# Performance work log

Measured on AMD Instinct MI355X. Metric: run time of the kernel, lower is better.

The kernel has to match this reference:

```python
import jax, jax.numpy as jnp
import numpy as np

N_NODES = 100000
N_EDGES = 1000000
HID = 128


def setup_inputs() -> dict:
    key = jax.random.key(0)
    ks = jax.random.split(key, 6)
    x = jax.random.normal(ks[0], (N_NODES, HID), dtype=jnp.float32)
    edge_index = jax.random.randint(ks[1], (2, N_EDGES), 0, N_NODES, dtype=jnp.int32)
    edge_attr = jax.random.uniform(ks[2], (N_EDGES, 1), dtype=jnp.float32)
    # MLP params (PyTorch Linear default-ish init scale)
    d_in = 2 * HID + 1  # 257
    W1 = jax.random.normal(ks[3], (d_in, HID), dtype=jnp.float32) / np.sqrt(d_in)
    b1 = jnp.zeros((HID,), dtype=jnp.float32)
    W2 = jax.random.normal(ks[4], (HID, 32), dtype=jnp.float32) / np.sqrt(HID)
    b2 = jnp.zeros((32,), dtype=jnp.float32)
    W3 = jax.random.normal(ks[5], (32, 1), dtype=jnp.float32) / np.sqrt(32.0)
    b3 = jnp.zeros((1,), dtype=jnp.float32)
    return {"x": x, "edge_index": edge_index, "edge_attr": edge_attr,
            "W1": W1, "b1": b1, "W2": W2, "b2": b2, "W3": W3, "b3": b3}


def reference(x, edge_index, edge_attr, W1, b1, W2, b2, W3, b3):
    src = edge_index[0]
    dst = edge_index[1]
    # [E, 2*H+1] gather + concat
    ef = jnp.concatenate([x[src], x[dst], edge_attr], axis=1)
    h = jax.nn.relu(ef @ W1 + b1)          # [E, H] (dropout = identity in eval)
    h = jax.nn.relu(h @ W2 + b2)           # [E, 32]
    out = jax.nn.sigmoid(h @ W3 + b3)      # [E, 1]
    return out[:, 0]                        # [E]
```

## Files before the change

kernel.cpp:

```cpp
#include <hip/hip_runtime.h>

#define E_EDGES 1000000
#define NNODES  100000
#define HID     128
#define NG      31250
#define NBLK    768
#define NT      62500
#define EBLK    1536
#define PBLK    512

typedef float f32x4 __attribute__((ext_vector_type(4)));
typedef short s16x8 __attribute__((ext_vector_type(8)));

typedef __attribute__((address_space(3))) unsigned int lds_u32;
typedef const __attribute__((address_space(1))) unsigned int glb_u32;

__device__ __forceinline__ void gl_lds16(const void* g, void* l) {
  __builtin_amdgcn_global_load_lds((glb_u32*)g, (lds_u32*)l, 16, 0, 0);
}

__device__ __forceinline__ unsigned short f2bf(float f) {
  unsigned int u = __float_as_uint(f);
  u += 0x7FFFu + ((u >> 16) & 1u);
  return (unsigned short)(u >> 16);
}

__device__ __forceinline__ unsigned int cvtpk_bf16(float lo, float hi) {
  unsigned int r;
  asm("v_cvt_pk_bf16_f32 %0, %1, %2" : "=v"(r) : "v"(lo), "v"(hi));
  return r;
}

__device__ __forceinline__ float bflo(unsigned int u) {
  return __uint_as_float(u << 16);
}
__device__ __forceinline__ float bfhi(unsigned int u) {
  return __uint_as_float(u & 0xffff0000u);
}

__device__ __forceinline__ int4 pack8(float4 a, float4 b) {
  int4 v;
  v.x = (int)((unsigned)f2bf(a.x) | ((unsigned)f2bf(a.y) << 16));
  v.y = (int)((unsigned)f2bf(a.z) | ((unsigned)f2bf(a.w) << 16));
  v.z = (int)((unsigned)f2bf(b.x) | ((unsigned)f2bf(b.y) << 16));
  v.w = (int)((unsigned)f2bf(b.z) | ((unsigned)f2bf(b.w) << 16));
  return v;
}

__global__ void cast_x_kernel(const float* __restrict__ x,
                              unsigned short* __restrict__ xb) {
  int i = blockIdx.x * blockDim.x + threadIdx.x;
  const float4* p = (const float4*)x;
  float4 a = p[2 * i];
  float4 b = p[2 * i + 1];
  int4 v = pack8(a, b);
  ((int4*)xb)[i] = v;
}

__global__ void edge_naive(const float* __restrict__ x, const int* __restrict__ ei,
                           const float* __restrict__ attr, const float* __restrict__ W1,
                           const float* __restrict__ b1, const float* __restrict__ W2,
                           const float* __restrict__ b2, const float* __restrict__ W3,
                           const float* __restrict__ b3, float* __restrict__ out) {
  const int e = blockIdx.x * blockDim.x + threadIdx.x;
  if (e >= E_EDGES) return;
  const float* xs = x + (size_t)ei[e] * HID;
  const float* xd = x + (size_t)ei[E_EDGES + e] * HID;
  const float a = attr[e];
  float h1[HID];
  for (int n = 0; n < HID; ++n) {
    float s = b1[n] + a * W1[256 * HID + n];
    for (int k = 0; k < HID; ++k)
      s += xs[k] * W1[k * HID + n] + xd[k] * W1[(128 + k) * HID + n];
    h1[n] = fmaxf(s, 0.f);
  }
  float o = b3[0];
  for (int n2 = 0; n2 < 32; ++n2) {
    float s = b2[n2];
    for (int n = 0; n < HID; ++n) s += h1[n] * W2[n * 32 + n2];
    o += fmaxf(s, 0.f) * W3[n2];
  }
  out[e] = 1.f / (1.f + __expf(-o));
}

__launch_bounds__(256, 3)
__global__ void edge_mlp_kernel(const unsigned short* __restrict__ xb,
                                const int* __restrict__ ei,
                                const float* __restrict__ attr,
                                const float* __restrict__ W1,
                                const float* __restrict__ b1,
                                const float* __restrict__ W2,
                                const float* __restrict__ b2,
                                const float* __restrict__ W3,
                                const float* __restrict__ b3,
                                float* __restrict__ out) {
  __shared__ __align__(16) unsigned char ef[2][16384];
  __shared__ __align__(16) unsigned char h1b[2][8704];
  __shared__ float red[2][4][16];

  const int tid  = threadIdx.x;
  const int w    = tid >> 6;
  const int lane = tid & 63;
  const int q    = lane >> 4;
  const int l15  = lane & 15;

  s16x8 B1[2][8];
  float b1v[2], w1l[2];
#pragma unroll
  for (int th = 0; th < 2; ++th) {
    const int nc = w * 32 + th * 16 + l15;
#pragma unroll
    for (int s = 0; s < 8; ++s)
#pragma unroll
      for (int j = 0; j < 8; ++j)
        B1[th][s][j] = (short)f2bf(W1[(s * 32 + q * 8 + j) * HID + nc]);
    b1v[th] = b1[nc];
    w1l[th] = W1[256 * HID + nc];
  }
  const int n2 = (w & 1) * 16 + l15;
  s16x8 B2[4];
#pragma unroll
  for (int s2 = 0; s2 < 4; ++s2)
#pragma unroll
    for (int j = 0; j < 8; ++j) {
      const int e = s2 * 32 + q * 8 + j;
      const int n = (e >> 5) * 32 + (e & 1) * 16 + ((e >> 1) & 15);
      B2[s2][j] = (short)f2bf(W2[n * 32 + n2]);
    }
  const float b2v = b2[n2];
  const float w3v = W3[n2];
  const float b3v = b3[0];

  const int bx = blockIdx.x;
  int nidA[4] = {0, 0, 0, 0}, nidB[4] = {0, 0, 0, 0};
  const int itmax = (NG - 1 - bx) / NBLK + 2;

  {
#pragma unroll
    for (int i = 0; i < 4; ++i) {
      const int f = w * 4 + i;
      nidA[i] = ei[(f >> 3) * E_EDGES + bx * 32 + (f & 7) * 4 + q];
    }
#pragma unroll
    for (int i = 0; i < 4; ++i) {
      const int f = w * 4 + i, m = (f & 7) * 4 + q;
      gl_lds16(xb + (size_t)nidA[i] * HID + ((l15 ^ (m & 7)) << 3),
               &ef[0][f * 1024]);
    }
    const int g1 = bx + NBLK;
    if (g1 < NG) {
#pragma unroll
      for (int i = 0; i < 4; ++i) {
        const int f = w * 4 + i;
        nidB[i] = ei[(f >> 3) * E_EDGES + g1 * 32 + (f & 7) * 4 + q];
      }
    }
  }
  __syncthreads();

#define ITER(IT, P, NIDU, NIDL)                                               \
  {                                                                           \
    const int g   = bx + (IT) * NBLK;                                         \
    const int g1  = g + NBLK;                                                 \
    const int g2  = g + 2 * NBLK;                                             \
    const int gm1 = g - NBLK;                                                 \
    const int gm2 = g - 2 * NBLK;                                             \
    if (g1 < NG) {                                                            \
      _Pragma("unroll") for (int i = 0; i < 4; ++i) {                         \
        const int f = w * 4 + i, m = (f & 7) * 4 + q;                         \
        gl_lds16(xb + (size_t)NIDU[i] * HID + ((l15 ^ (m & 7)) << 3),         \
                 &ef[(P) ^ 1][f * 1024]);                                     \
      }                                                                       \
    }                                                                         \
    if (g2 < NG) {                                                            \
      _Pragma("unroll") for (int i = 0; i < 4; ++i) {                         \
        const int f = w * 4 + i;                                              \
        NIDL[i] = ei[(f >> 3) * E_EDGES + g2 * 32 + (f & 7) * 4 + q];         \
      }                                                                       \
    }                                                                         \
    if (g < NG) {                                                             \
      const f32x4 at0 = *(const f32x4*)(attr + g * 32 + q * 4);               \
      const f32x4 at1 = *(const f32x4*)(attr + g * 32 + 16 + q * 4);          \
      _Pragma("unroll") for (int t = 0; t < 2; ++t) {                         \
        f32x4 a0 = {0.f, 0.f, 0.f, 0.f}, a1 = {0.f, 0.f, 0.f, 0.f};          \
        _Pragma("unroll") for (int s = 0; s < 8; ++s) {                       \
          const int ch = s * 4 + q;                                           \
          const s16x8 A = *(const s16x8*)&ef[P][(ch >> 4) * 8192 + t * 4096   \
              + l15 * 256 + (((ch & 15) ^ (l15 & 7)) << 4)];                  \
          a0 = __builtin_amdgcn_mfma_f32_16x16x32_bf16(A, B1[0][s], a0, 0, 0, 0); \
          a1 = __builtin_amdgcn_mfma_f32_16x16x32_bf16(A, B1[1][s], a1, 0, 0, 0); \
        }                                                                     \
        const f32x4 at = t ? at1 : at0;                                       \
        _Pragma("unroll") for (int r = 0; r < 4; ++r) {                       \
          const float v0 = fmaxf(a0[r] + b1v[0] + at[r] * w1l[0], 0.f);       \
          const float v1 = fmaxf(a1[r] + b1v[1] + at[r] * w1l[1], 0.f);       \
          const unsigned int pk =                                             \
              (unsigned)f2bf(v0) | ((unsigned)f2bf(v1) << 16);                \
          *(unsigned int*)&h1b[P][t * 4352 + (q * 4 + r) * 272                \
                                  + (w * 16 + l15) * 4] = pk;                 \
        }                                                                     \
      }                                                                       \
    }                                                                         \
    if (gm1 >= 0 && gm1 < NG) {                                               \
      const int t = w >> 1;                                                   \
      f32x4 c0 = {0.f, 0.f, 0.f, 0.f};                                        \
      _Pragma("unroll") for (int s2 = 0; s2 < 4; ++s2) {                      \
        const s16x8 A2 = *(const s16x8*)&h1b[(P) ^ 1][t * 4352 + l15 * 272    \
                                                      + s2 * 64 + q * 16];    \
        c0 = __builtin_amdgcn_mfma_f32_16x16x32_bf16(A2, B2[s2], c0, 0, 0, 0); \
      }                                                                       \
      float p0 = fmaxf(c0[0] + b2v, 0.f) * w3v;                               \
      float p1 = fmaxf(c0[1] + b2v, 0.f) * w3v;                               \
      float p2 = fmaxf(c0[2] + b2v, 0.f) * w3v;                               \
      float p3 = fmaxf(c0[3] + b2v, 0.f) * w3v;                               \
      _Pragma("unroll") for (int off = 8; off >= 1; off >>= 1) {              \
        p0 += __shfl_xor(p0, off, 16);                                        \
        p1 += __shfl_xor(p1, off, 16);                                        \
        p2 += __shfl_xor(p2, off, 16);                                        \
        p3 += __shfl_xor(p3, off, 16);                                        \
      }                                                                       \
      if (l15 == 0) {                                                         \
        red[P][w][q * 4 + 0] = p0;                                            \
        red[P][w][q * 4 + 1] = p1;                                            \
        red[P][w][q * 4 + 2] = p2;                                            \
        red[P][w][q * 4 + 3] = p3;                                            \
      }                                                                       \
    }                                                                         \
    if (gm2 >= 0 && tid < 32) {                                               \
      const int tt = tid >> 4, mm = tid & 15;                                 \
      const float sv = red[(P) ^ 1][tt * 2][mm]                               \
                     + red[(P) ^ 1][tt * 2 + 1][mm] + b3v;                    \
      out[gm2 * 32 + tid] = 1.f / (1.f + __expf(-sv));                        \
    }                                                                         \
    __syncthreads();                                                          \
  }

  for (int itb = 0;; itb += 2) {
    ITER(itb, 0, nidB, nidA)
    if (itb >= itmax) break;
    ITER(itb + 1, 1, nidA, nidB)
    if (itb + 1 >= itmax) break;
  }
#undef ITER
}

__launch_bounds__(256, 2)
__global__ void node_precompute(const float* __restrict__ x,
                                const float* __restrict__ W1,
                                const float* __restrict__ b1,
                                unsigned int* __restrict__ Pa,
                                unsigned int* __restrict__ Pb) {
  __shared__ __align__(16) unsigned char xs[32 * 272];
  const int tid = threadIdx.x;
  const int w = tid >> 6, lane = tid & 63, q = lane >> 4, l15 = lane & 15;
  const int side = w >> 1;
  const int cb   = (w & 1) * 64;

  s16x8 Bf[4][4];
  float bh[4];
#pragma unroll
  for (int nt = 0; nt < 4; ++nt) {
    const int c = cb + nt * 16 + l15;
    bh[nt] = 0.5f * b1[c];
#pragma unroll
    for (int s = 0; s < 4; ++s)
#pragma unroll
      for (int j = 0; j < 8; ++j)
        Bf[nt][s][j] = (short)f2bf(W1[(side * 128 + s * 32 + q * 8 + j) * HID + c]);
  }
  unsigned int* const dstP = side ? Pb : Pa;

  for (int tile = blockIdx.x; tile < NNODES / 32; tile += gridDim.x) {
    const int n0 = tile * 32;
    {
      const int r = tid >> 3, cc = tid & 7;
      const float* src = x + (size_t)(n0 + r) * HID + cc * 16;
      float4 f0 = ((const float4*)src)[0];
      float4 f1 = ((const float4*)src)[1];
      float4 f2 = ((const float4*)src)[2];
      float4 f3 = ((const float4*)src)[3];
      *(int4*)&xs[r * 272 + cc * 32]      = pack8(f0, f1);
      *(int4*)&xs[r * 272 + cc * 32 + 16] = pack8(f2, f3);
    }
    __syncthreads();

#pragma unroll
    for (int mt = 0; mt < 2; ++mt) {
      s16x8 A[4];
#pragma unroll
      for (int s = 0; s < 4; ++s)
        A[s] = *(const s16x8*)&xs[(mt * 16 + l15) * 272 + (s * 4 + q) * 16];
      f32x4 acc[4];
#pragma unroll
      for (int nt = 0; nt < 4; ++nt) {
        acc[nt] = (f32x4){0.f, 0.f, 0.f, 0.f};
#pragma unroll
        for (int s = 0; s < 4; ++s)
          acc[nt] = __builtin_amdgcn_mfma_f32_16x16x32_bf16(A[s], Bf[nt][s], acc[nt], 0, 0, 0);
      }
#pragma unroll
      for (int p = 0; p < 2; ++p)
#pragma unroll
        for (int r = 0; r < 4; ++r) {
          const int node = n0 + mt * 16 + q * 4 + r;
          const unsigned int pk = cvtpk_bf16(acc[2 * p][r] + bh[2 * p],
                                             acc[2 * p + 1][r] + bh[2 * p + 1]);
          dstP[(size_t)node * 64 + (w & 1) * 32 + p * 16 + l15] = pk;
        }
    }
    __syncthreads();
  }
}

__launch_bounds__(256, 3)
__global__ void edge_mlp2(const unsigned int* __restrict__ Pa,
                          const unsigned int* __restrict__ Pb,
                          const int* __restrict__ ei,
                          const float* __restrict__ attr,
                          const float* __restrict__ W1,
                          const float* __restrict__ W2,
                          const float* __restrict__ b2,
                          const float* __restrict__ W3,
                          const float* __restrict__ b3,
                          float* __restrict__ out) {
  const int tid = threadIdx.x;
  const int w = tid >> 6, lane = tid & 63, q = lane >> 4, l15 = lane & 15;
  const int wid = blockIdx.x * 4 + w;
  const int nw  = EBLK * 4;

  s16x8 B2a[4], B2b[4];
#pragma unroll
  for (int s = 0; s < 4; ++s)
#pragma unroll
    for (int j = 0; j < 8; ++j) {
      const int n = s * 32 + q * 4 + (j >> 1) + ((j & 1) << 4);
      B2a[s][j] = (short)f2bf(W2[n * 32 + l15]);
      B2b[s][j] = (short)f2bf(W2[n * 32 + 16 + l15]);
    }
  int4 w1p[4];
#pragma unroll
  for (int s = 0; s < 4; ++s) {
    unsigned int uu[4];
#pragma unroll
    for (int m = 0; m < 4; ++m) {
      const int n = s * 32 + q * 4 + m;
      uu[m] = (unsigned)f2bf(W1[256 * HID + n]) |
              ((unsigned)f2bf(W1[256 * HID + n + 16]) << 16);
    }
    w1p[s] = make_int4((int)uu[0], (int)uu[1], (int)uu[2], (int)uu[3]);
  }
  const float b2a = b2[l15], b2b = b2[16 + l15];
  const float w3a = W3[l15], w3b = W3[16 + l15];
  const float b3v = b3[0];

  int t = wid;
  if (t >= NT) return;

#define IDS(T, SID, DID, AT)                                                  \
  {                                                                           \
    const int tt_ = (T) < NT ? (T) : NT - 1;                                  \
    SID = ei[tt_ * 16 + l15];                                                 \
    DID = ei[E_EDGES + tt_ * 16 + l15];                                       \
    AT  = attr[tt_ * 16 + l15];                                               \
  }

#define GATH(GA, GB, SID, DID)                                                \
  {                                                                           \
    const unsigned int* pa_ = Pa + (size_t)(SID) * 64;                        \
    const unsigned int* pb_ = Pb + (size_t)(DID) * 64;                        \
    _Pragma("unroll") for (int s = 0; s < 4; ++s)                             \
        GA[s] = *(const int4*)(pa_ + s * 16 + q * 4);                         \
    _Pragma("unroll") for (int s = 0; s < 4; ++s)                             \
        GB[s] = *(const int4*)(pb_ + s * 16 + q * 4);                         \
  }

#define COMP(T, GA, GB, ATV)                                                  \
  {                                                                           \
    f32x4 c0 = {0.f, 0.f, 0.f, 0.f}, c1 = {0.f, 0.f, 0.f, 0.f};              \
    _Pragma("unroll") for (int s = 0; s < 4; ++s) {                           \
      const unsigned int* ua = (const unsigned int*)&GA[s];                   \
      const unsigned int* ub = (const unsigned int*)&GB[s];                   \
      const unsigned int* uw = (const unsigned int*)&w1p[s];                  \
      int4 afi;                                                               \
      unsigned int* af = (unsigned int*)&afi;                                 \
      _Pragma("unroll") for (int m = 0; m < 4; ++m) {                         \
        float v0 = bflo(ua[m]) + bflo(ub[m]) + (ATV) * bflo(uw[m]);           \
        float v1 = bfhi(ua[m]) + bfhi(ub[m]) + (ATV) * bfhi(uw[m]);           \
        v0 = fmaxf(v0, 0.f);                                                  \
        v1 = fmaxf(v1, 0.f);                                                  \
        af[m] = cvtpk_bf16(v0, v1);                                           \
      }                                                                       \
      const s16x8 A_ = *(const s16x8*)&afi;                                   \
      c0 = __builtin_amdgcn_mfma_f32_16x16x32_bf16(A_, B2a[s], c0, 0, 0, 0);  \
      c1 = __builtin_amdgcn_mfma_f32_16x16x32_bf16(A_, B2b[s], c1, 0, 0, 0);  \
    }                                                                         \
    float p0 = fmaxf(c0[0] + b2a, 0.f) * w3a + fmaxf(c1[0] + b2b, 0.f) * w3b; \
    float p1 = fmaxf(c0[1] + b2a, 0.f) * w3a + fmaxf(c1[1] + b2b, 0.f) * w3b; \
    float p2 = fmaxf(c0[2] + b2a, 0.f) * w3a + fmaxf(c1[2] + b2b, 0.f) * w3b; \
    float p3 = fmaxf(c0[3] + b2a, 0.f) * w3a + fmaxf(c1[3] + b2b, 0.f) * w3b; \
    _Pragma("unroll") for (int off = 8; off >= 1; off >>= 1) {                \
      p0 += __shfl_xor(p0, off, 16);                                          \
      p1 += __shfl_xor(p1, off, 16);                                          \
      p2 += __shfl_xor(p2, off, 16);                                          \
      p3 += __shfl_xor(p3, off, 16);                                          \
    }                                                                         \
    if (l15 == 0) {                                                           \
      float4 o4;                                                              \
      o4.x = 1.f / (1.f + __expf(-(p0 + b3v)));                               \
      o4.y = 1.f / (1.f + __expf(-(p1 + b3v)));                               \
      o4.z = 1.f / (1.f + __expf(-(p2 + b3v)));                               \
      o4.w = 1.f / (1.f + __expf(-(p3 + b3v)));                               \
      *(float4*)&out[(T) * 16 + q * 4] = o4;                                  \
    }                                                                         \
  }

  int4 ga0[4], gb0[4], ga1[4], gb1[4];
  int sid, did;
  float at0, at1, atN;

  IDS(t, sid, did, at0);
  GATH(ga0, gb0, sid, did);
  IDS(t + nw, sid, did, atN);

  while (true) {
    const int t1 = t + nw;
    GATH(ga1, gb1, sid, did);
    at1 = atN;
    IDS(t1 + nw, sid, did, atN);
    COMP(t, ga0, gb0, at0);
    if (t1 >= NT) break;

    const int t2 = t1 + nw;
    GATH(ga0, gb0, sid, did);
    at0 = atN;
    IDS(t2 + nw, sid, did, atN);
    COMP(t1, ga1, gb1, at1);
    if (t2 >= NT) break;

    t = t2;
  }
#undef IDS
#undef GATH
#undef COMP
}

extern "C" void kernel_launch(void* const* d_in, const int* in_sizes, int n_in,
                              void* d_out, int out_size, void* d_ws, size_t ws_size,
                              hipStream_t stream) {
  const float* x    = (const float*)d_in[0];
  const int*   ei   = (const int*)d_in[1];
  const float* attr = (const float*)d_in[2];
  const float* W1   = (const float*)d_in[3];
  const float* b1   = (const float*)d_in[4];
  const float* W2   = (const float*)d_in[5];
  const float* b2   = (const float*)d_in[6];
  const float* W3   = (const float*)d_in[7];
  const float* b3   = (const float*)d_in[8];
  float* out = (float*)d_out;

  const size_t needP = (size_t)NNODES * HID * 2 * sizeof(unsigned short);
  const size_t need1 = (size_t)NNODES * HID * sizeof(unsigned short);
  if (ws_size >= needP) {
    unsigned int* Pa = (unsigned int*)d_ws;
    unsigned int* Pb = Pa + (size_t)NNODES * 64;
    node_precompute<<<PBLK, 256, 0, stream>>>(x, W1, b1, Pa, Pb);
    edge_mlp2<<<EBLK, 256, 0, stream>>>(Pa, Pb, ei, attr, W1, W2, b2, W3, b3, out);
  } else if (ws_size >= need1) {
    unsigned short* xb = (unsigned short*)d_ws;
    cast_x_kernel<<<6250, 256, 0, stream>>>(x, xb);
    edge_mlp_kernel<<<NBLK, 256, 0, stream>>>(xb, ei, attr, W1, b1, W2, b2, W3, b3, out);
  } else {
    edge_naive<<<(E_EDGES + 255) / 256, 256, 0, stream>>>(x, ei, attr, W1, b1, W2, b2, W3, b3, out);
  }
}
```

Baseline: 187.4 us.

## Quantize per-node layer-1 projections to int8 with per-row scales for edge gather

The node precompute kernel now stores the W1 projections of each node as 8-bit values with a per-node absmax scale instead of bf16, using an LDS staging pass to compute the scales and permute columns. The edge kernel gathers half as many bytes per endpoint plus two scale floats, and dequantizes with byte-to-float conversions fused into FMAs before the ReLU and layer-2 MFMA. The aim is to cut the random-gather memory traffic that dominates the edge kernel. In exchange it adds reduction and LDS work in precompute and lowers precision of the hidden activations.

```diff
diff --git a/kernel.cpp b/kernel.cpp
--- a/kernel.cpp
+++ b/kernel.cpp
@@ -36,6 +36,19 @@
 }
 __device__ __forceinline__ float bfhi(unsigned int u) {
   return __uint_as_float(u & 0xffff0000u);
+}
+
+__device__ __forceinline__ float cvub0(unsigned int u) {
+  float r; asm("v_cvt_f32_ubyte0 %0, %1" : "=v"(r) : "v"(u)); return r;
+}
+__device__ __forceinline__ float cvub1(unsigned int u) {
+  float r; asm("v_cvt_f32_ubyte1 %0, %1" : "=v"(r) : "v"(u)); return r;
+}
+__device__ __forceinline__ float cvub2(unsigned int u) {
+  float r; asm("v_cvt_f32_ubyte2 %0, %1" : "=v"(r) : "v"(u)); return r;
+}
+__device__ __forceinline__ float cvub3(unsigned int u) {
+  float r; asm("v_cvt_f32_ubyte3 %0, %1" : "=v"(r) : "v"(u)); return r;
 }
 
 __device__ __forceinline__ int4 pack8(float4 a, float4 b) {
@@ -245,16 +258,21 @@
 }
 
 __launch_bounds__(256, 2)
-__global__ void node_precompute(const float* __restrict__ x,
-                                const float* __restrict__ W1,
-                                const float* __restrict__ b1,
-                                unsigned int* __restrict__ Pa,
-                                unsigned int* __restrict__ Pb) {
+__global__ void node_precompute8(const float* __restrict__ x,
+                                 const float* __restrict__ W1,
+                                 const float* __restrict__ b1,
+                                 unsigned char* __restrict__ P8a,
+                                 unsigned char* __restrict__ P8b,
+                                 float* __restrict__ Sa,
+                                 float* __restrict__ Sb) {
   __shared__ __align__(16) unsigned char xs[32 * 272];
+  __shared__ float pvf[2][32][132];
+  __shared__ float sclh[2][2][32];
+  __shared__ float sinv[2][32];
   const int tid = threadIdx.x;
   const int w = tid >> 6, lane = tid & 63, q = lane >> 4, l15 = lane & 15;
-  const int side = w >> 1;
-  const int cb   = (w & 1) * 64;
+  const int sd = w >> 1;
+  const int cb = (w & 1) * 64;
 
   s16x8 Bf[4][4];
   float bh[4];
@@ -266,9 +284,8 @@
     for (int s = 0; s < 4; ++s)
 #pragma unroll
       for (int j = 0; j < 8; ++j)
-        Bf[nt][s][j] = (short)f2bf(W1[(side * 128 + s * 32 + q * 8 + j) * HID + c]);
-  }
-  unsigned int* const dstP = side ? Pb : Pa;
+        Bf[nt][s][j] = (short)f2bf(W1[(sd * 128 + s * 32 + q * 8 + j) * HID + c]);
+  }
 
   for (int tile = blockIdx.x; tile < NNODES / 32; tile += gridDim.x) {
     const int n0 = tile * 32;
@@ -290,31 +307,78 @@
 #pragma unroll
       for (int s = 0; s < 4; ++s)
         A[s] = *(const s16x8*)&xs[(mt * 16 + l15) * 272 + (s * 4 + q) * 16];
-      f32x4 acc[4];
+      float pv[4][4];
 #pragma unroll
       for (int nt = 0; nt < 4; ++nt) {
-        acc[nt] = (f32x4){0.f, 0.f, 0.f, 0.f};
+        f32x4 acc = {0.f, 0.f, 0.f, 0.f};
 #pragma unroll
         for (int s = 0; s < 4; ++s)
-          acc[nt] = __builtin_amdgcn_mfma_f32_16x16x32_bf16(A[s], Bf[nt][s], acc[nt], 0, 0, 0);
+          acc = __builtin_amdgcn_mfma_f32_16x16x32_bf16(A[s], Bf[nt][s], acc, 0, 0, 0);
+#pragma unroll
+        for (int r = 0; r < 4; ++r) pv[nt][r] = acc[r] + bh[nt];
       }
 #pragma unroll
-      for (int p = 0; p < 2; ++p)
-#pragma unroll
-        for (int r = 0; r < 4; ++r) {
-          const int node = n0 + mt * 16 + q * 4 + r;
-          const unsigned int pk = cvtpk_bf16(acc[2 * p][r] + bh[2 * p],
-                                             acc[2 * p + 1][r] + bh[2 * p + 1]);
-          dstP[(size_t)node * 64 + (w & 1) * 32 + p * 16 + l15] = pk;
+      for (int nt = 0; nt < 4; ++nt)
+#pragma unroll
+        for (int r = 0; r < 4; ++r)
+          pvf[sd][mt * 16 + q * 4 + r][cb + nt * 16 + l15] = pv[nt][r];
+      float m4[4];
+#pragma unroll
+      for (int r = 0; r < 4; ++r)
+        m4[r] = fmaxf(fmaxf(fabsf(pv[0][r]), fabsf(pv[1][r])),
+                      fmaxf(fabsf(pv[2][r]), fabsf(pv[3][r])));
+#pragma unroll
+      for (int off = 8; off >= 1; off >>= 1)
+#pragma unroll
+        for (int r = 0; r < 4; ++r)
+          m4[r] = fmaxf(m4[r], __shfl_xor(m4[r], off, 16));
+      if (l15 == 0) {
+#pragma unroll
+        for (int r = 0; r < 4; ++r)
+          sclh[sd][w & 1][mt * 16 + q * 4 + r] = m4[r];
+      }
+    }
+    __syncthreads();
+
+    if (tid < 64) {
+      const int sdd = tid >> 5, row = tid & 31;
+      const float m = fmaxf(sclh[sdd][0][row], sclh[sdd][1][row]);
+      (sdd ? Sb : Sa)[n0 + row] = m * (1.f / 127.f);
+      sinv[sdd][row] = m > 0.f ? 127.f / m : 0.f;
+    }
+    __syncthreads();
+
+    {
+      const int rg = tid >> 2, part = tid & 3;
+      const int sdd = rg >> 5, row = rg & 31;
+      const float inv = sinv[sdd][row];
+      unsigned int dw[8];
+#pragma unroll
+      for (int bi = 0; bi < 8; ++bi) {
+        unsigned int u32v = 0;
+#pragma unroll
+        for (int bb = 0; bb < 4; ++bb) {
+          const int p = part * 32 + bi * 4 + bb;
+          const int col = ((p >> 6) * 2 + ((p >> 3) & 1)) * 32
+                          + ((p >> 4) & 3) * 8 + (p & 7);
+          const int u = (int)rintf(pvf[sdd][row][col] * inv) + 128;
+          u32v |= ((unsigned)u & 0xffu) << (8 * bb);
         }
+        dw[bi] = u32v;
+      }
+      unsigned char* dst = (sdd ? P8b : P8a) + (size_t)(n0 + row) * 128 + part * 32;
+      *(int4*)dst        = make_int4((int)dw[0], (int)dw[1], (int)dw[2], (int)dw[3]);
+      *(int4*)(dst + 16) = make_int4((int)dw[4], (int)dw[5], (int)dw[6], (int)dw[7]);
     }
     __syncthreads();
   }
 }
 
 __launch_bounds__(256, 3)
-__global__ void edge_mlp2(const unsigned int* __restrict__ Pa,
-                          const unsigned int* __restrict__ Pb,
+__global__ void edge_mlp3(const unsigned char* __restrict__ P8a,
+                          const unsigned char* __restrict__ P8b,
+                          const float* __restrict__ Sa,
+                          const float* __restrict__ Sb,
                           const int* __restrict__ ei,
                           const float* __restrict__ attr,
                           const float* __restrict__ W1,
@@ -333,9 +397,9 @@
   for (int s = 0; s < 4; ++s)
 #pragma unroll
     for (int j = 0; j < 8; ++j) {
-      const int n = s * 32 + q * 4 + (j >> 1) + ((j & 1) << 4);
-      B2a[s][j] = (short)f2bf(W2[n * 32 + l15]);
-      B2b[s][j] = (short)f2bf(W2[n * 32 + 16 + l15]);
+      const int k = s * 32 + q * 8 + j;
+      B2a[s][j] = (short)f2bf(W2[k * 32 + l15]);
+      B2b[s][j] = (short)f2bf(W2[k * 32 + 16 + l15]);
     }
   int4 w1p[4];
 #pragma unroll
@@ -343,9 +407,9 @@
     unsigned int uu[4];
 #pragma unroll
     for (int m = 0; m < 4; ++m) {
-      const int n = s * 32 + q * 4 + m;
-      uu[m] = (unsigned)f2bf(W1[256 * HID + n]) |
-              ((unsigned)f2bf(W1[256 * HID + n + 16]) << 16);
+      const int k = s * 32 + q * 8 + 2 * m;
+      uu[m] = (unsigned)f2bf(W1[256 * HID + k]) |
+              ((unsigned)f2bf(W1[256 * HID + k + 1]) << 16);
     }
     w1p[s] = make_int4((int)uu[0], (int)uu[1], (int)uu[2], (int)uu[3]);
   }
@@ -364,31 +428,44 @@
     AT  = attr[tt_ * 16 + l15];                                               \
   }
 
-#define GATH(GA, GB, SID, DID)                                                \
+#define GATH(LA, LB, SAv, SBv, SID, DID)                                      \
   {                                                                           \
-    const unsigned int* pa_ = Pa + (size_t)(SID) * 64;                        \
-    const unsigned int* pb_ = Pb + (size_t)(DID) * 64;                        \
-    _Pragma("unroll") for (int s = 0; s < 4; ++s)                             \
-        GA[s] = *(const int4*)(pa_ + s * 16 + q * 4);                         \
-    _Pragma("unroll") for (int s = 0; s < 4; ++s)                             \
-        GB[s] = *(const int4*)(pb_ + s * 16 + q * 4);                         \
-  }
-
-#define COMP(T, GA, GB, ATV)                                                  \
+    const unsigned char* pa_ = P8a + (size_t)(SID) * 128 + q * 16;            \
+    const unsigned char* pb_ = P8b + (size_t)(DID) * 128 + q * 16;            \
+    LA[0] = *(const int4*)pa_;                                                \
+    LA[1] = *(const int4*)(pa_ + 64);                                         \
+    LB[0] = *(const int4*)pb_;                                                \
+    LB[1] = *(const int4*)(pb_ + 64);                                         \
+    SAv = Sa[SID];                                                            \
+    SBv = Sb[DID];                                                            \
+  }
+
+#define COMP(T, LA, LB, SAv, SBv, ATV)                                        \
   {                                                                           \
+    const float kq = -128.f * ((SAv) + (SBv));                                \
     f32x4 c0 = {0.f, 0.f, 0.f, 0.f}, c1 = {0.f, 0.f, 0.f, 0.f};              \
     _Pragma("unroll") for (int s = 0; s < 4; ++s) {                           \
-      const unsigned int* ua = (const unsigned int*)&GA[s];                   \
-      const unsigned int* ub = (const unsigned int*)&GB[s];                   \
+      const int* la_ = (const int*)&LA[s >> 1];                               \
+      const int* lb_ = (const int*)&LB[s >> 1];                               \
       const unsigned int* uw = (const unsigned int*)&w1p[s];                  \
       int4 afi;                                                               \
       unsigned int* af = (unsigned int*)&afi;                                 \
-      _Pragma("unroll") for (int m = 0; m < 4; ++m) {                         \
-        float v0 = bflo(ua[m]) + bflo(ub[m]) + (ATV) * bflo(uw[m]);           \
-        float v1 = bfhi(ua[m]) + bfhi(ub[m]) + (ATV) * bfhi(uw[m]);           \
-        v0 = fmaxf(v0, 0.f);                                                  \
-        v1 = fmaxf(v1, 0.f);                                                  \
-        af[m] = cvtpk_bf16(v0, v1);                                           \
+      _Pragma("unroll") for (int dd = 0; dd < 2; ++dd) {                      \
+        const unsigned int ua = (unsigned int)la_[(s & 1) * 2 + dd];          \
+        const unsigned int ub = (unsigned int)lb_[(s & 1) * 2 + dd];          \
+        const unsigned int w0 = uw[2 * dd], w1_ = uw[2 * dd + 1];             \
+        float v0 = fmaf((SAv), cvub0(ua),                                     \
+                        fmaf((SBv), cvub0(ub), fmaf((ATV), bflo(w0), kq)));   \
+        float v1 = fmaf((SAv), cvub1(ua),                                     \
+                        fmaf((SBv), cvub1(ub), fmaf((ATV), bfhi(w0), kq)));   \
+        float v2 = fmaf((SAv), cvub2(ua),                                     \
+                        fmaf((SBv), cvub2(ub), fmaf((ATV), bflo(w1_), kq)));  \
+        float v3 = fmaf((SAv), cvub3(ua),                                     \
+                        fmaf((SBv), cvub3(ub), fmaf((ATV), bfhi(w1_), kq)));  \
+        v0 = fmaxf(v0, 0.f); v1 = fmaxf(v1, 0.f);                             \
+        v2 = fmaxf(v2, 0.f); v3 = fmaxf(v3, 0.f);                             \
+        af[2 * dd]     = cvtpk_bf16(v0, v1);                                  \
+        af[2 * dd + 1] = cvtpk_bf16(v2, v3);                                  \
       }                                                                       \
       const s16x8 A_ = *(const s16x8*)&afi;                                   \
       c0 = __builtin_amdgcn_mfma_f32_16x16x32_bf16(A_, B2a[s], c0, 0, 0, 0);  \
@@ -414,27 +491,27 @@
     }                                                                         \
   }
 
-  int4 ga0[4], gb0[4], ga1[4], gb1[4];
+  int4 La0[2], Lb0[2], La1[2], Lb1[2];
   int sid, did;
-  float at0, at1, atN;
-
-  IDS(t, sid, did, at0);
-  GATH(ga0, gb0, sid, did);
+  float sa0, sb0, sa1, sb1, at0v, at1v, atN;
+
+  IDS(t, sid, did, at0v);
+  GATH(La0, Lb0, sa0, sb0, sid, did);
   IDS(t + nw, sid, did, atN);
 
   while (true) {
     const int t1 = t + nw;
-    GATH(ga1, gb1, sid, did);
-    at1 = atN;
+    GATH(La1, Lb1, sa1, sb1, sid, did);
+    at1v = atN;
     IDS(t1 + nw, sid, did, atN);
-    COMP(t, ga0, gb0, at0);
+    COMP(t, La0, Lb0, sa0, sb0, at0v);
     if (t1 >= NT) break;
 
     const int t2 = t1 + nw;
-    GATH(ga0, gb0, sid, did);
-    at0 = atN;
+    GATH(La0, Lb0, sa0, sb0, sid, did);
+    at0v = atN;
     IDS(t2 + nw, sid, did, atN);
-    COMP(t1, ga1, gb1, at1);
+    COMP(t1, La1, Lb1, sa1, sb1, at1v);
     if (t2 >= NT) break;
 
     t = t2;
@@ -458,13 +535,15 @@
   const float* b3   = (const float*)d_in[8];
   float* out = (float*)d_out;
 
-  const size_t needP = (size_t)NNODES * HID * 2 * sizeof(unsigned short);
+  const size_t need8 = (size_t)NNODES * 256 + (size_t)NNODES * 8;
   const size_t need1 = (size_t)NNODES * HID * sizeof(unsigned short);
-  if (ws_size >= needP) {
-    unsigned int* Pa = (unsigned int*)d_ws;
-    unsigned int* Pb = Pa + (size_t)NNODES * 64;
-    node_precompute<<<PBLK, 256, 0, stream>>>(x, W1, b1, Pa, Pb);
-    edge_mlp2<<<EBLK, 256, 0, stream>>>(Pa, Pb, ei, attr, W1, W2, b2, W3, b3, out);
+  if (ws_size >= need8) {
+    unsigned char* P8a = (unsigned char*)d_ws;
+    unsigned char* P8b = P8a + (size_t)NNODES * 128;
+    float* Sa = (float*)(P8a + (size_t)NNODES * 256);
+    float* Sb = Sa + NNODES;
+    node_precompute8<<<PBLK, 256, 0, stream>>>(x, W1, b1, P8a, P8b, Sa, Sb);
+    edge_mlp3<<<EBLK, 256, 0, stream>>>(P8a, P8b, Sa, Sb, ei, attr, W1, W2, b2, W3, b3, out);
   } else if (ws_size >= need1) {
     unsigned short* xb = (unsigned short*)d_ws;
     cast_x_kernel<<<6250, 256, 0, stream>>>(x, xb);
```

After: 168.9 us. 1.11x faster.
